# Kernel optimization log

Measured on AMD Instinct MI355X. Metric: run time of the kernel, lower is better.

Reference implementation:

```python
import jax, jax.numpy as jnp
import numpy as np

STAGES = [80, 40, 20]
INPUT = 640
NUM_CLASSES = 80
B = 32
PRE_NMS = 1000      # top-k candidates fed to NMS (fixed-shape surrogate for full sort)
MAX_DET = 100       # max_num_detections
IOU_TH = 0.5
CLASS_OFF = 4096.0  # batched_nms trick: offset boxes per class so classes never overlap


def setup_inputs() -> dict:
    key = jax.random.key(0)
    ks = jax.random.split(key, 6)
    inp = {}
    for i, s in enumerate(STAGES):
        inp[f"cls{i}"] = jax.random.normal(ks[2 * i], (B, NUM_CLASSES, s, s), dtype=jnp.float32)
        # positive ltrb distances, up to ~64 px
        inp[f"box{i}"] = jax.random.uniform(ks[2 * i + 1], (B, 4, s, s), dtype=jnp.float32) * 64.0
    return inp


def _decode_level(cls, box, stage):
    # cls: [B,C,H,W], box: [B,4,H,W]
    step = INPUT // stage
    cls = jax.nn.sigmoid(jnp.transpose(cls, (0, 2, 3, 1)))   # [B,H,W,C]
    conf = jnp.max(cls, axis=-1)                             # [B,H,W]
    cidx = jnp.argmax(cls, axis=-1)                          # [B,H,W]
    box = jnp.transpose(box, (0, 2, 3, 1))                   # [B,H,W,4]
    grid = jnp.arange(stage, dtype=box.dtype) * step
    gx, gy = jnp.meshgrid(grid, grid, indexing='xy')
    block = jnp.stack([gx, gy], axis=-1)                     # [H,W,2]
    xy1 = block - box[..., :2]
    xy2 = block + box[..., 2:4]
    boxes = jnp.concatenate([xy1, xy2], axis=-1).reshape(box.shape[0], -1, 4)
    return boxes, conf.reshape(conf.shape[0], -1), cidx.reshape(cidx.shape[0], -1)


def _iou_matrix(b):
    # b: [N,4] -> [N,N] pairwise IoU
    area = jnp.maximum(b[:, 2] - b[:, 0], 0.) * jnp.maximum(b[:, 3] - b[:, 1], 0.)
    lt = jnp.maximum(b[:, None, :2], b[None, :, :2])
    rb = jnp.minimum(b[:, None, 2:], b[None, :, 2:])
    wh = jnp.maximum(rb - lt, 0.)
    inter = wh[..., 0] * wh[..., 1]
    return inter / (area[:, None] + area[None, :] - inter + 1e-7)


def _nms_image(boxes, scores, classes):
    # class-aware (batched) NMS via per-class coordinate offset
    off = classes.astype(boxes.dtype) * CLASS_OFF
    ob = boxes + off[:, None]
    s_top, idx = jax.lax.top_k(scores, PRE_NMS)
    b_top = ob[idx]                                          # [PRE,4], score-sorted desc
    iou = _iou_matrix(b_top)
    ar = jnp.arange(PRE_NMS)

    def body(i, supp):
        row = (iou[i] > IOU_TH) & (ar > i)
        return jnp.where(supp[i], supp, supp | row)

    supp = jax.lax.fori_loop(0, PRE_NMS, body, jnp.zeros((PRE_NMS,), bool))
    kept_scores = jnp.where(supp, -jnp.inf, s_top)
    sel_s, sel = jax.lax.top_k(kept_scores, MAX_DET)
    final = idx[sel]                                         # indices into original 8400
    valid = jnp.isfinite(sel_s)
    out_b = jnp.where(valid[:, None], boxes[final], 0.)
    out_s = jnp.where(valid, scores[final], 0.)
    out_c = jnp.where(valid, classes[final], -1)
    return out_b, out_s, out_c


def reference(cls0, box0, cls1, box1, cls2, box2):
    parts = [_decode_level(c, b, s) for c, b, s in
             zip([cls0, cls1, cls2], [box0, box1, box2], STAGES)]
    boxes = jnp.concatenate([p[0] for p in parts], axis=1)    # [B,8400,4]
    scores = jnp.concatenate([p[1] for p in parts], axis=1)   # [B,8400]
    classes = jnp.concatenate([p[2] for p in parts], axis=1)  # [B,8400]
    ob, os_, oc = jax.vmap(_nms_image)(boxes, scores, classes)
    boxes_with_scores = jnp.concatenate([ob, os_[..., None]], axis=-1)  # [B,MAX_DET,5]
    return boxes_with_scores, oc
```

## Files before the change

kernel.cpp:

```cpp
#include <hip/hip_runtime.h>

typedef unsigned int u32;
typedef unsigned long long u64;

#define NB 32
#define NCLS 80
#define NANCHOR 8400
#define PRE 1000
#define MAXDET 100
#define NT 1024

__global__ void decode_kernel(const float* __restrict__ cls0, const float* __restrict__ box0,
                              const float* __restrict__ cls1, const float* __restrict__ box1,
                              const float* __restrict__ cls2, const float* __restrict__ box2,
                              float* __restrict__ ws_scores, float4* __restrict__ ws_boxes,
                              int* __restrict__ ws_cls) {
    int g = blockIdx.x * blockDim.x + threadIdx.x;
    if (g >= NB * NANCHOR) return;
    int b = g / NANCHOR;
    int r = g - b * NANCHOR;

    const float* cp; const float* bp;
    int HW, hw, h, w, step;
    if (r < 6400) {
        cp = cls0 + (size_t)b * NCLS * 6400; bp = box0 + (size_t)b * 4 * 6400;
        HW = 6400; hw = r;        h = hw / 80; w = hw - h * 80; step = 8;
    } else if (r < 8000) {
        cp = cls1 + (size_t)b * NCLS * 1600; bp = box1 + (size_t)b * 4 * 1600;
        HW = 1600; hw = r - 6400; h = hw / 40; w = hw - h * 40; step = 16;
    } else {
        cp = cls2 + (size_t)b * NCLS * 400;  bp = box2 + (size_t)b * 4 * 400;
        HW = 400;  hw = r - 8000; h = hw / 20; w = hw - h * 20; step = 32;
    }

    float m = cp[hw];
    int ci = 0;
    for (int c = 1; c < NCLS; ++c) {
        float v = cp[(size_t)c * HW + hw];
        if (v > m) { m = v; ci = c; }
    }
    float score = 1.0f / (1.0f + expf(-m));

    float l = bp[hw], t = bp[HW + hw], rr = bp[2 * HW + hw], bo = bp[3 * HW + hw];
    float gx = (float)(w * step), gy = (float)(h * step);

    ws_scores[g] = score;
    ws_boxes[g] = make_float4(gx - l, gy - t, gx + rr, gy + bo);
    ws_cls[g] = ci;
}

__global__ __launch_bounds__(NT) void nms_kernel(const float* __restrict__ ws_scores,
                                                 const float4* __restrict__ ws_boxes,
                                                 const int* __restrict__ ws_cls,
                                                 float* __restrict__ out) {
    const int b = blockIdx.x;
    const int tid = threadIdx.x;

    __shared__ int s_hist[1024];
    __shared__ u64 s_key[2048];
    __shared__ float s_x1[PRE], s_y1[PRE], s_x2[PRE], s_y2[PRE], s_area[PRE];
    __shared__ int s_supp[PRE];
    __shared__ int s_keep[MAXDET];
    __shared__ int s_C, s_base;
    __shared__ u32 s_thresh;
    __shared__ int s_cnt;

    const float* sc = ws_scores + (size_t)b * NANCHOR;

    s_hist[tid] = 0;
    __syncthreads();
    for (int a = tid; a < NANCHOR; a += NT) {
        u32 sb = __float_as_uint(sc[a]);
        atomicAdd(&s_hist[sb >> 20], 1);
    }
    __syncthreads();
    for (int off = 1; off < 1024; off <<= 1) {
        int v = s_hist[tid];
        int u = (tid + off < 1024) ? s_hist[tid + off] : 0;
        __syncthreads();
        s_hist[tid] = v + u;
        __syncthreads();
    }
    {
        int sfx = s_hist[tid];
        int nxt = (tid < 1023) ? s_hist[tid + 1] : 0;
        if (sfx >= PRE && (tid == 1023 || nxt < PRE)) { s_C = tid; s_base = nxt; }
    }
    __syncthreads();
    const int C = s_C, base = s_base;
    __syncthreads();

    s_hist[tid] = 0;
    __syncthreads();
    for (int a = tid; a < NANCHOR; a += NT) {
        u32 sb = __float_as_uint(sc[a]);
        if ((int)(sb >> 20) == C) atomicAdd(&s_hist[(sb >> 10) & 1023], 1);
    }
    __syncthreads();
    for (int off = 1; off < 1024; off <<= 1) {
        int v = s_hist[tid];
        int u = (tid + off < 1024) ? s_hist[tid + off] : 0;
        __syncthreads();
        s_hist[tid] = v + u;
        __syncthreads();
    }
    {
        int sfx = base + s_hist[tid];
        int nxt = base + ((tid < 1023) ? s_hist[tid + 1] : 0);
        if (sfx >= PRE && (tid == 1023 || nxt < PRE))
            s_thresh = ((u32)C << 20) | ((u32)tid << 10);
    }
    if (tid == 0) s_cnt = 0;
    s_key[tid] = 0ULL;
    s_key[tid + 1024] = 0ULL;
    __syncthreads();
    const u32 thresh = s_thresh;

    for (int a = tid; a < NANCHOR; a += NT) {
        u32 sb = __float_as_uint(sc[a]);
        if (sb >= thresh) {
            int pos = atomicAdd(&s_cnt, 1);
            if (pos < 2048)
                s_key[pos] = ((u64)sb << 14) | (u64)(NANCHOR - 1 - a);
        }
    }
    __syncthreads();

    for (int k = 2; k <= 2048; k <<= 1) {
        for (int j = k >> 1; j > 0; j >>= 1) {
            for (int i = tid; i < 2048; i += NT) {
                int ixj = i ^ j;
                if (ixj > i) {
                    u64 va = s_key[i], vb = s_key[ixj];
                    bool desc = ((i & k) == 0);
                    if (desc ? (va < vb) : (va > vb)) { s_key[i] = vb; s_key[ixj] = va; }
                }
            }
            __syncthreads();
        }
    }

    if (tid < PRE) {
        u64 key = s_key[tid];
        int idx = (NANCHOR - 1) - (int)(key & 16383ULL);
        float4 bx = ws_boxes[(size_t)b * NANCHOR + idx];
        int c = ws_cls[(size_t)b * NANCHOR + idx];
        float off = (float)c * 4096.0f;
        float x1 = bx.x + off, y1 = bx.y + off, x2 = bx.z + off, y2 = bx.w + off;
        s_x1[tid] = x1; s_y1[tid] = y1; s_x2[tid] = x2; s_y2[tid] = y2;
        s_area[tid] = fmaxf(x2 - x1, 0.0f) * fmaxf(y2 - y1, 0.0f);
        s_supp[tid] = 0;
    }
    __syncthreads();

    int nkept = 0;
    for (int i = 0; i < PRE; ++i) {
        if (s_supp[i]) continue;
        if (tid == 0) s_keep[nkept] = i;
        nkept++;
        if (nkept >= MAXDET) break;
        float xi1 = s_x1[i], yi1 = s_y1[i], xi2 = s_x2[i], yi2 = s_y2[i], ai = s_area[i];
        int j = i + 1 + tid;
        if (j < PRE && !s_supp[j]) {
            float lx = fmaxf(xi1, s_x1[j]);
            float ly = fmaxf(yi1, s_y1[j]);
            float rx = fminf(xi2, s_x2[j]);
            float ry = fminf(yi2, s_y2[j]);
            float wx = fmaxf(rx - lx, 0.0f);
            float wy = fmaxf(ry - ly, 0.0f);
            float inter = wx * wy;
            float iou = inter / (ai + s_area[j] - inter + 1e-7f);
            if (iou > 0.5f) s_supp[j] = 1;
        }
        __syncthreads();
    }
    __syncthreads();

    if (tid < MAXDET) {
        float* o = out + ((size_t)b * MAXDET + tid) * 5;
        float* oc = out + (size_t)NB * MAXDET * 5 + (size_t)b * MAXDET + tid;
        if (tid < nkept) {
            int i = s_keep[tid];
            u64 key = s_key[i];
            int idx = (NANCHOR - 1) - (int)(key & 16383ULL);
            float score = __uint_as_float((u32)(key >> 14));
            float4 bx = ws_boxes[(size_t)b * NANCHOR + idx];
            int c = ws_cls[(size_t)b * NANCHOR + idx];
            o[0] = bx.x; o[1] = bx.y; o[2] = bx.z; o[3] = bx.w; o[4] = score;
            *oc = (float)c;
        } else {
            o[0] = 0.0f; o[1] = 0.0f; o[2] = 0.0f; o[3] = 0.0f; o[4] = 0.0f;
            *oc = -1.0f;
        }
    }
}

extern "C" void kernel_launch(void* const* d_in, const int* in_sizes, int n_in,
                              void* d_out, int out_size, void* d_ws, size_t ws_size,
                              hipStream_t stream) {
    const float* cls0 = (const float*)d_in[0];
    const float* box0 = (const float*)d_in[1];
    const float* cls1 = (const float*)d_in[2];
    const float* box1 = (const float*)d_in[3];
    const float* cls2 = (const float*)d_in[4];
    const float* box2 = (const float*)d_in[5];

    float* ws = (float*)d_ws;
    float* ws_scores = ws;
    float4* ws_boxes = (float4*)(ws + NB * NANCHOR);
    int* ws_cls = (int*)(ws + (size_t)NB * NANCHOR * 5);

    int total = NB * NANCHOR;
    decode_kernel<<<(total + 255) / 256, 256, 0, stream>>>(
        cls0, box0, cls1, box1, cls2, box2, ws_scores, ws_boxes, ws_cls);

    nms_kernel<<<NB, NT, 0, stream>>>(ws_scores, ws_boxes, ws_cls, (float*)d_out);
}
```

Measured before the change: 205.6 us.

## Split top-k selection from NMS and run suppression in one register-resident wave

The single NMS kernel becomes two kernels. A 1024-thread select kernel builds per-wave histograms, uses wave-shuffle suffix scans and ballot-aggregated compaction, and ranks candidates by counting instead of a bitonic sort. It writes the sorted, class-offset boxes into the workspace in place of the consumed scores. A 64-thread NMS kernel then keeps each lane's 16 candidate boxes in registers and tracks suppression as a bitmask exchanged by shuffles, removing the per-iteration block-wide barriers of the greedy loop. The cost is an extra launch, a quadratic rank count over roughly 1000 keys, and a serial greedy loop that now runs on a single wave.

```diff
diff --git a/kernel.cpp b/kernel.cpp
--- a/kernel.cpp
+++ b/kernel.cpp
@@ -8,7 +8,7 @@
 #define NANCHOR 8400
 #define PRE 1000
 #define MAXDET 100
-#define NT 1024
+
 
 __global__ void decode_kernel(const float* __restrict__ cls0, const float* __restrict__ box0,
                               const float* __restrict__ cls1, const float* __restrict__ box1,
@@ -49,148 +49,208 @@
     ws_cls[g] = ci;
 }
 
-__global__ __launch_bounds__(NT) void nms_kernel(const float* __restrict__ ws_scores,
+__device__ __forceinline__ int wave_suffix_incl(int v, int lane) {
+    #pragma unroll
+    for (int off = 1; off < 64; off <<= 1) {
+        int t = __shfl_down(v, off);
+        if (lane + off < 64) v += t;
+    }
+    return v;
+}
+
+__global__ __launch_bounds__(1024) void select_kernel(float* ws,
+                                                      const float4* __restrict__ ws_boxes,
+                                                      const int* __restrict__ ws_cls) {
+    const int b = blockIdx.x;
+    const int tid = threadIdx.x;
+    const int lane = tid & 63;
+    const int wv = tid >> 6;
+
+    __shared__ int s_hist[4][1024];
+    __shared__ u64 s_key[2048];
+    __shared__ int s_wtot[16];
+    __shared__ int s_C, s_base, s_cnt;
+    __shared__ u32 s_thresh;
+
+    const float* sc = ws + (size_t)b * NANCHOR;
+    float4* sbox = (float4*)(ws + (size_t)b * NANCHOR);
+    u64*    skey = (u64*)(ws + (size_t)b * NANCHOR + 4096);
+    float*  sarea = ws + (size_t)b * NANCHOR + 6144;
+
+    u32 sb[9];
+    #pragma unroll
+    for (int k = 0; k < 9; ++k) {
+        int a = tid + (k << 10);
+        sb[k] = (a < NANCHOR) ? __float_as_uint(sc[a]) : 0u;
+    }
+    int* hp = &s_hist[0][0];
+    hp[tid] = 0; hp[tid + 1024] = 0; hp[tid + 2048] = 0; hp[tid + 3072] = 0;
+    if (tid == 0) s_cnt = 0;
+    __syncthreads();
+
+    #pragma unroll
+    for (int k = 0; k < 9; ++k) {
+        int a = tid + (k << 10);
+        if (a < NANCHOR) atomicAdd(&s_hist[wv & 3][sb[k] >> 20], 1);
+    }
+    __syncthreads();
+    {
+        int v = s_hist[0][tid] + s_hist[1][tid] + s_hist[2][tid] + s_hist[3][tid];
+        int wincl = wave_suffix_incl(v, lane);
+        if (lane == 0) s_wtot[wv] = wincl;
+        __syncthreads();
+        int add = 0;
+        #pragma unroll
+        for (int w = 0; w < 16; ++w) if (w > wv) add += s_wtot[w];
+        int sfx = wincl + add;
+        int nxt = sfx - v;
+        if (sfx >= PRE && nxt < PRE) { s_C = tid; s_base = nxt; }
+        hp[tid] = 0; hp[tid + 1024] = 0; hp[tid + 2048] = 0; hp[tid + 3072] = 0;
+    }
+    __syncthreads();
+    const int C = s_C, base0 = s_base;
+
+    #pragma unroll
+    for (int k = 0; k < 9; ++k) {
+        int a = tid + (k << 10);
+        if (a < NANCHOR && (int)(sb[k] >> 20) == C)
+            atomicAdd(&s_hist[wv & 3][(sb[k] >> 10) & 1023], 1);
+    }
+    __syncthreads();
+    {
+        int v = s_hist[0][tid] + s_hist[1][tid] + s_hist[2][tid] + s_hist[3][tid];
+        int wincl = wave_suffix_incl(v, lane);
+        if (lane == 0) s_wtot[wv] = wincl;
+        __syncthreads();
+        int add = 0;
+        #pragma unroll
+        for (int w = 0; w < 16; ++w) if (w > wv) add += s_wtot[w];
+        int sfx = wincl + add;
+        int nxt = sfx - v;
+        if (base0 + sfx >= PRE && base0 + nxt < PRE)
+            s_thresh = ((u32)C << 20) | ((u32)tid << 10);
+    }
+    __syncthreads();
+    const u32 T = s_thresh;
+
+    #pragma unroll
+    for (int k = 0; k < 9; ++k) {
+        int a = tid + (k << 10);
+        bool pred = (a < NANCHOR) && (sb[k] >= T);
+        u64 mask = __ballot(pred);
+        if (pred) {
+            int leader = __ffsll(mask) - 1;
+            int bpos = 0;
+            if (lane == leader) bpos = atomicAdd(&s_cnt, __popcll(mask));
+            bpos = __shfl(bpos, leader);
+            int pos = bpos + __popcll(mask & ((1ULL << lane) - 1ULL));
+            if (pos < 2048)
+                s_key[pos] = ((u64)sb[k] << 14) | (u64)(NANCHOR - 1 - a);
+        }
+    }
+    __syncthreads();
+
+    int cnt = s_cnt; if (cnt > 2048) cnt = 2048;
+    for (int slot = tid; slot < cnt; slot += 1024) {
+        u64 me = s_key[slot];
+        int rank = 0;
+        int y = 0;
+        for (; y + 4 <= cnt; y += 4) {
+            rank += (int)(s_key[y] > me) + (int)(s_key[y + 1] > me)
+                  + (int)(s_key[y + 2] > me) + (int)(s_key[y + 3] > me);
+        }
+        for (; y < cnt; ++y) rank += (int)(s_key[y] > me);
+        if (rank < PRE) {
+            int idx = (NANCHOR - 1) - (int)(me & 16383ULL);
+            float4 bx = ws_boxes[(size_t)b * NANCHOR + idx];
+            int c = ws_cls[(size_t)b * NANCHOR + idx];
+            float off = (float)c * 4096.0f;
+            float x1 = bx.x + off, y1 = bx.y + off, x2 = bx.z + off, y2 = bx.w + off;
+            sbox[rank] = make_float4(x1, y1, x2, y2);
+            sarea[rank] = fmaxf(x2 - x1, 0.0f) * fmaxf(y2 - y1, 0.0f);
+            skey[rank] = me;
+        }
+    }
+}
+
+__global__ __launch_bounds__(64) void nms_kernel(const float* __restrict__ ws,
                                                  const float4* __restrict__ ws_boxes,
                                                  const int* __restrict__ ws_cls,
                                                  float* __restrict__ out) {
     const int b = blockIdx.x;
-    const int tid = threadIdx.x;
-
-    __shared__ int s_hist[1024];
-    __shared__ u64 s_key[2048];
-    __shared__ float s_x1[PRE], s_y1[PRE], s_x2[PRE], s_y2[PRE], s_area[PRE];
-    __shared__ int s_supp[PRE];
+    const int lane = threadIdx.x;
+
+    const float4* sbox = (const float4*)(ws + (size_t)b * NANCHOR);
+    const u64*    skey = (const u64*)(ws + (size_t)b * NANCHOR + 4096);
+    const float*  sarea = ws + (size_t)b * NANCHOR + 6144;
+
+    __shared__ float4 s_box[PRE];
+    __shared__ float s_area[PRE];
     __shared__ int s_keep[MAXDET];
-    __shared__ int s_C, s_base;
-    __shared__ u32 s_thresh;
-    __shared__ int s_cnt;
-
-    const float* sc = ws_scores + (size_t)b * NANCHOR;
-
-    s_hist[tid] = 0;
-    __syncthreads();
-    for (int a = tid; a < NANCHOR; a += NT) {
-        u32 sb = __float_as_uint(sc[a]);
-        atomicAdd(&s_hist[sb >> 20], 1);
-    }
-    __syncthreads();
-    for (int off = 1; off < 1024; off <<= 1) {
-        int v = s_hist[tid];
-        int u = (tid + off < 1024) ? s_hist[tid + off] : 0;
-        __syncthreads();
-        s_hist[tid] = v + u;
-        __syncthreads();
-    }
-    {
-        int sfx = s_hist[tid];
-        int nxt = (tid < 1023) ? s_hist[tid + 1] : 0;
-        if (sfx >= PRE && (tid == 1023 || nxt < PRE)) { s_C = tid; s_base = nxt; }
-    }
-    __syncthreads();
-    const int C = s_C, base = s_base;
-    __syncthreads();
-
-    s_hist[tid] = 0;
-    __syncthreads();
-    for (int a = tid; a < NANCHOR; a += NT) {
-        u32 sb = __float_as_uint(sc[a]);
-        if ((int)(sb >> 20) == C) atomicAdd(&s_hist[(sb >> 10) & 1023], 1);
-    }
-    __syncthreads();
-    for (int off = 1; off < 1024; off <<= 1) {
-        int v = s_hist[tid];
-        int u = (tid + off < 1024) ? s_hist[tid + off] : 0;
-        __syncthreads();
-        s_hist[tid] = v + u;
-        __syncthreads();
-    }
-    {
-        int sfx = base + s_hist[tid];
-        int nxt = base + ((tid < 1023) ? s_hist[tid + 1] : 0);
-        if (sfx >= PRE && (tid == 1023 || nxt < PRE))
-            s_thresh = ((u32)C << 20) | ((u32)tid << 10);
-    }
-    if (tid == 0) s_cnt = 0;
-    s_key[tid] = 0ULL;
-    s_key[tid + 1024] = 0ULL;
-    __syncthreads();
-    const u32 thresh = s_thresh;
-
-    for (int a = tid; a < NANCHOR; a += NT) {
-        u32 sb = __float_as_uint(sc[a]);
-        if (sb >= thresh) {
-            int pos = atomicAdd(&s_cnt, 1);
-            if (pos < 2048)
-                s_key[pos] = ((u64)sb << 14) | (u64)(NANCHOR - 1 - a);
-        }
-    }
-    __syncthreads();
-
-    for (int k = 2; k <= 2048; k <<= 1) {
-        for (int j = k >> 1; j > 0; j >>= 1) {
-            for (int i = tid; i < 2048; i += NT) {
-                int ixj = i ^ j;
-                if (ixj > i) {
-                    u64 va = s_key[i], vb = s_key[ixj];
-                    bool desc = ((i & k) == 0);
-                    if (desc ? (va < vb) : (va > vb)) { s_key[i] = vb; s_key[ixj] = va; }
-                }
-            }
-            __syncthreads();
-        }
-    }
-
-    if (tid < PRE) {
-        u64 key = s_key[tid];
-        int idx = (NANCHOR - 1) - (int)(key & 16383ULL);
-        float4 bx = ws_boxes[(size_t)b * NANCHOR + idx];
-        int c = ws_cls[(size_t)b * NANCHOR + idx];
-        float off = (float)c * 4096.0f;
-        float x1 = bx.x + off, y1 = bx.y + off, x2 = bx.z + off, y2 = bx.w + off;
-        s_x1[tid] = x1; s_y1[tid] = y1; s_x2[tid] = x2; s_y2[tid] = y2;
-        s_area[tid] = fmaxf(x2 - x1, 0.0f) * fmaxf(y2 - y1, 0.0f);
-        s_supp[tid] = 0;
-    }
-    __syncthreads();
-
+
+    float jx1[16], jy1[16], jx2[16], jy2[16], ja[16];
+    #pragma unroll
+    for (int k = 0; k < 16; ++k) {
+        int j = lane + (k << 6);
+        if (j < PRE) {
+            float4 v = sbox[j];
+            float a = sarea[j];
+            s_box[j] = v; s_area[j] = a;
+            jx1[k] = v.x; jy1[k] = v.y; jx2[k] = v.z; jy2[k] = v.w; ja[k] = a;
+        } else {
+            jx1[k] = 3.0e8f; jy1[k] = 3.0e8f; jx2[k] = 3.0e8f; jy2[k] = 3.0e8f;
+            ja[k] = 0.0f;
+        }
+    }
+    __syncthreads();
+
+    u32 supp = 0;
     int nkept = 0;
     for (int i = 0; i < PRE; ++i) {
-        if (s_supp[i]) continue;
-        if (tid == 0) s_keep[nkept] = i;
+        int owner = i & 63, kk = i >> 6;
+        u32 um = (u32)__shfl((int)supp, owner);
+        if ((um >> kk) & 1) continue;
+        if (lane == 0) s_keep[nkept] = i;
         nkept++;
         if (nkept >= MAXDET) break;
-        float xi1 = s_x1[i], yi1 = s_y1[i], xi2 = s_x2[i], yi2 = s_y2[i], ai = s_area[i];
-        int j = i + 1 + tid;
-        if (j < PRE && !s_supp[j]) {
-            float lx = fmaxf(xi1, s_x1[j]);
-            float ly = fmaxf(yi1, s_y1[j]);
-            float rx = fminf(xi2, s_x2[j]);
-            float ry = fminf(yi2, s_y2[j]);
+        float4 bi = s_box[i];
+        float ai = s_area[i];
+        #pragma unroll
+        for (int k = 0; k < 16; ++k) {
+            int j = lane + (k << 6);
+            bool act = (j > i) && (j < PRE) && !((supp >> k) & 1);
+            float lx = fmaxf(bi.x, jx1[k]);
+            float ly = fmaxf(bi.y, jy1[k]);
+            float rx = fminf(bi.z, jx2[k]);
+            float ry = fminf(bi.w, jy2[k]);
             float wx = fmaxf(rx - lx, 0.0f);
             float wy = fmaxf(ry - ly, 0.0f);
             float inter = wx * wy;
-            float iou = inter / (ai + s_area[j] - inter + 1e-7f);
-            if (iou > 0.5f) s_supp[j] = 1;
-        }
-        __syncthreads();
-    }
-    __syncthreads();
-
-    if (tid < MAXDET) {
-        float* o = out + ((size_t)b * MAXDET + tid) * 5;
-        float* oc = out + (size_t)NB * MAXDET * 5 + (size_t)b * MAXDET + tid;
-        if (tid < nkept) {
-            int i = s_keep[tid];
-            u64 key = s_key[i];
-            int idx = (NANCHOR - 1) - (int)(key & 16383ULL);
-            float score = __uint_as_float((u32)(key >> 14));
-            float4 bx = ws_boxes[(size_t)b * NANCHOR + idx];
-            int c = ws_cls[(size_t)b * NANCHOR + idx];
-            o[0] = bx.x; o[1] = bx.y; o[2] = bx.z; o[3] = bx.w; o[4] = score;
-            *oc = (float)c;
-        } else {
-            o[0] = 0.0f; o[1] = 0.0f; o[2] = 0.0f; o[3] = 0.0f; o[4] = 0.0f;
-            *oc = -1.0f;
+            float den = ai + ja[k] - inter + 1e-7f;
+            if (act && (inter > 0.5f * den)) supp |= (1u << k);
+        }
+    }
+    __syncthreads();
+
+    #pragma unroll
+    for (int t = 0; t < 2; ++t) {
+        int r = lane + (t << 6);
+        if (r < MAXDET) {
+            float* o = out + ((size_t)b * MAXDET + r) * 5;
+            float* oc = out + (size_t)NB * MAXDET * 5 + (size_t)b * MAXDET + r;
+            if (r < nkept) {
+                int i = s_keep[r];
+                u64 key = skey[i];
+                int idx = (NANCHOR - 1) - (int)(key & 16383ULL);
+                float score = __uint_as_float((u32)(key >> 14));
+                float4 bx = ws_boxes[(size_t)b * NANCHOR + idx];
+                int c = ws_cls[(size_t)b * NANCHOR + idx];
+                o[0] = bx.x; o[1] = bx.y; o[2] = bx.z; o[3] = bx.w; o[4] = score;
+                *oc = (float)c;
+            } else {
+                o[0] = 0.0f; o[1] = 0.0f; o[2] = 0.0f; o[3] = 0.0f; o[4] = 0.0f;
+                *oc = -1.0f;
+            }
         }
     }
 }
@@ -214,5 +274,7 @@
     decode_kernel<<<(total + 255) / 256, 256, 0, stream>>>(
         cls0, box0, cls1, box1, cls2, box2, ws_scores, ws_boxes, ws_cls);
 
-    nms_kernel<<<NB, NT, 0, stream>>>(ws_scores, ws_boxes, ws_cls, (float*)d_out);
-}
+    select_kernel<<<NB, 1024, 0, stream>>>(ws, ws_boxes, ws_cls);
+
+    nms_kernel<<<NB, 64, 0, stream>>>(ws, ws_boxes, ws_cls, (float*)d_out);
+}
```

Result: slower. 275.7 us (+34.1%).
